# Kernel optimization log

Hardware: AMD Instinct MI355X
Metric: run time of the kernel (lower is better)

Reference implementation:

```python
import jax, jax.numpy as jnp
from jax import lax
import numpy as np

# FlowNetC correlation configuration (matches init_kwargs)
PAD = 20          # pad_size
K = 1             # kernel_size (kernel_radius = 0)
MAX_DISP = 20     # max_displacement
S1 = 1            # stride1
S2 = 2            # stride2
R = MAX_DISP // S2          # neighborhood_grid_radius = 10
GW = 2 * R + 1              # neighborhood_grid_width = 21
NOUT = GW * GW              # 441 output planes


def setup_inputs() -> dict:
    key = jax.random.key(0)
    k1, k2 = jax.random.split(key)
    B, C, H, W = 8, 256, 96, 128
    return {
        "input1": jax.random.normal(k1, (B, C, H, W), dtype=jnp.float32),
        "input2": jax.random.normal(k2, (B, C, H, W), dtype=jnp.float32),
    }


def _correlation(input1, input2):
    B, C, H, W = input1.shape
    # pad second input; with kernel_size=1 and pad==max_displacement the
    # output grid is exactly the input grid, and displaced pixel (y+dy, x+dx)
    # lives at padded index (y + PAD + dy, x + PAD + dx).
    p2 = jnp.pad(input2, ((0, 0), (0, 0), (PAD, PAD), (PAD, PAD)))
    sumelems = jnp.asarray(K * K * C, dtype=input1.dtype)

    def body(o):
        # displacement (dy, dx) = ((o//GW - R)*S2, (o%GW - R)*S2);
        # slice start in padded coords = PAD + d = (o//GW)*S2, (o%GW)*S2
        dy = (o // GW) * S2
        dx = (o % GW) * S2
        sl = lax.dynamic_slice(p2, (0, 0, dy, dx), (B, C, H, W))
        return jnp.einsum('bchw,bchw->bhw', input1, sl) / sumelems

    out = lax.map(body, jnp.arange(NOUT))       # [441, B, H, W]
    return jnp.transpose(out, (1, 0, 2, 3))     # [B, 441, H, W]


def reference(input1, input2):
    return _correlation(input1, input2)
```

## Files before the change

### kernel.cpp

```cpp
#include <hip/hip_runtime.h>
#include <hip/hip_bf16.h>


typedef __attribute__((ext_vector_type(8))) short bf16x8;
typedef __attribute__((ext_vector_type(4))) float f32x4;
typedef __attribute__((ext_vector_type(4))) unsigned u32x4;

constexpr int Bn = 8, Cn = 256, Hn = 96, Wn = 128, GW = 21;
constexpr int KC = 32, NCH = Cn / KC;
constexpr int NWG = Bn * Hn * GW;
constexpr int JW = 23;
constexpr size_t TELEMS = (size_t)Bn * Hn * NCH * 2048;

__device__ inline unsigned pack_bf16(float lo, float hi) {
    __hip_bfloat16 l = __float2bfloat16(lo);
    __hip_bfloat16 h = __float2bfloat16(hi);
    unsigned short lu, hu;
    __builtin_memcpy(&lu, &l, 2);
    __builtin_memcpy(&hu, &h, 2);
    return (unsigned)lu | ((unsigned)hu << 16);
}

__global__ __launch_bounds__(256) void prepack(
    const float* __restrict__ in1, const float* __restrict__ in2,
    unsigned* __restrict__ T)
{
    unsigned u = blockIdx.x;
    int ch = u & 7;  u >>= 3;
    int y  = u % 96; u /= 96;
    int b  = u & 7;  u >>= 3;
    const float* src = u ? in2 : in1;

    int t  = threadIdx.x;
    int tm = t & 63;
    int tg = t >> 6;

    const size_t chw = (size_t)Hn * Wn;
    const float* p = src + ((size_t)(b * Cn + ch * 32 + 8 * tg)) * chw
                         + (size_t)y * Wn + 2 * tm;
    float2 f[8];
#pragma unroll
    for (int k = 0; k < 8; ++k)
        f[k] = *(const float2*)(p + (size_t)k * chw);

    u32x4 ae, ao;
#pragma unroll
    for (int ku = 0; ku < 4; ++ku) {
        ae[ku] = pack_bf16(f[2 * ku].x, f[2 * ku + 1].x);
        ao[ku] = pack_bf16(f[2 * ku].y, f[2 * ku + 1].y);
    }
    unsigned* To = T + u * TELEMS + ((size_t)(b * Hn + y) * NCH + ch) * 2048
                     + ((tm >> 4) * 4 + tg) * 64 + (tm & 15) * 4;
    *(u32x4*)(To)        = ae;
    *(u32x4*)(To + 1024) = ao;
}

__global__ __launch_bounds__(256) void corr_frag(
    const unsigned* __restrict__ T1, const unsigned* __restrict__ T2,
    float* __restrict__ out)
{
    __shared__ float sout[Wn * JW];

    int orig = blockIdx.x;
    int xcd  = orig & 7;
    int i    = orig >> 3;
    int yw   = i % 3;  int t = i / 3;
    int dyi  = t % 21; t /= 21;
    int sub  = t & 1;
    int par  = (t >> 1) & 1;
    int b    = t >> 2;
    int y    = 12 * xcd + par + 2 * (3 * sub + yw);

    int y2  = y + 2 * dyi - 20;
    bool y2ok = (y2 >= 0) && (y2 < Hn);

    int tid = threadIdx.x;
    int w   = tid >> 6;
    int l   = tid & 63;
    int p   = w >> 1;
    int h   = w & 1;
    int g   = l >> 4;
    int m16 = l & 15;

    f32x4 acc[2][4] = {};

    if (y2ok) {
        const unsigned* pa = T1 + (size_t)(b * Hn + y)  * (NCH * 2048)
                                + p * 1024 + g * 64 + m16 * 4;
        const unsigned* pb = T2 + (size_t)(b * Hn + y2) * (NCH * 2048)
                                + p * 1024 + g * 64 + m16 * 4 + h * 256;

        bf16x8 ca0, ca1, cb0, cb1, cb2;
        ca0 = *(const bf16x8*)(pa + (2 * h + 0) * 256);
        ca1 = *(const bf16x8*)(pa + (2 * h + 1) * 256);
        cb0 = *(const bf16x8*)(pb + 0 * 256);
        cb1 = *(const bf16x8*)(pb + 1 * 256);
        cb2 = *(const bf16x8*)(pb + 2 * 256);

        for (int ch = 0; ch < NCH; ++ch) {
            bf16x8 na0, na1, nb0, nb1, nb2;
            if (ch + 1 < NCH) {
                const unsigned* A = pa + (ch + 1) * 2048;
                const unsigned* B = pb + (ch + 1) * 2048;
                na0 = *(const bf16x8*)(A + (2 * h + 0) * 256);
                na1 = *(const bf16x8*)(A + (2 * h + 1) * 256);
                nb0 = *(const bf16x8*)(B + 0 * 256);
                nb1 = *(const bf16x8*)(B + 1 * 256);
                nb2 = *(const bf16x8*)(B + 2 * 256);
            }
            if (h == 0) {
                acc[0][0] = __builtin_amdgcn_mfma_f32_16x16x32_bf16(ca0, cb0, acc[0][0], 0, 0, 0);
                acc[0][1] = __builtin_amdgcn_mfma_f32_16x16x32_bf16(ca0, cb1, acc[0][1], 0, 0, 0);
                acc[1][0] = __builtin_amdgcn_mfma_f32_16x16x32_bf16(ca1, cb0, acc[1][0], 0, 0, 0);
                acc[1][1] = __builtin_amdgcn_mfma_f32_16x16x32_bf16(ca1, cb1, acc[1][1], 0, 0, 0);
                acc[1][2] = __builtin_amdgcn_mfma_f32_16x16x32_bf16(ca1, cb2, acc[1][2], 0, 0, 0);
            } else {
                acc[0][1] = __builtin_amdgcn_mfma_f32_16x16x32_bf16(ca0, cb0, acc[0][1], 0, 0, 0);
                acc[0][2] = __builtin_amdgcn_mfma_f32_16x16x32_bf16(ca0, cb1, acc[0][2], 0, 0, 0);
                acc[0][3] = __builtin_amdgcn_mfma_f32_16x16x32_bf16(ca0, cb2, acc[0][3], 0, 0, 0);
                acc[1][2] = __builtin_amdgcn_mfma_f32_16x16x32_bf16(ca1, cb1, acc[1][2], 0, 0, 0);
                acc[1][3] = __builtin_amdgcn_mfma_f32_16x16x32_bf16(ca1, cb2, acc[1][3], 0, 0, 0);
            }
            ca0 = na0; ca1 = na1;
            cb0 = nb0; cb1 = nb1; cb2 = nb2;
        }
    }

    for (int i2 = tid; i2 < Wn * JW; i2 += 256) sout[i2] = 0.0f;
    __syncthreads();

    if (y2ok) {
        const float scale = 1.0f / 256.0f;
#pragma unroll
        for (int a = 0; a < 2; ++a)
#pragma unroll
            for (int n = 0; n < 4; ++n)
#pragma unroll
                for (int r = 0; r < 4; ++r) {
                    int xp = (2 * h + a) * 16 + g * 4 + r;
                    int up = n * 16 + m16;
                    int j  = up - xp + 10;
                    if ((unsigned)j < 21u)
                        sout[(2 * xp + p) * JW + j] = acc[a][n][r] * scale;
                }
    }
    __syncthreads();

    unsigned base0 = (unsigned)(((b * (GW * GW) + dyi * GW) * Hn + y) * Wn);
    constexpr unsigned PLANE = (unsigned)(Hn * Wn);
    for (int s = tid; s < GW * Wn; s += 256) {
        int j = s >> 7;
        int x = s & 127;
        out[base0 + (unsigned)j * PLANE + (unsigned)x] = sout[x * JW + j];
    }
}

__device__ inline void lds_barrier() {
    asm volatile("s_waitcnt lgkmcnt(0)" ::: "memory");
    __builtin_amdgcn_s_barrier();
    __builtin_amdgcn_sched_barrier(0);
}

__global__ __launch_bounds__(256) void corr_mfma_fb(
    const float* __restrict__ in1, const float* __restrict__ in2,
    float* __restrict__ out)
{
    __shared__ unsigned lds[4][1024];
    int orig = blockIdx.x;
    int xcd  = orig & 7;
    int i    = orig >> 3;
    int yw   = i % 3;  int t = i / 3;
    int dyi  = t % 21; t /= 21;
    int sub  = t & 1;
    int par  = (t >> 1) & 1;
    int b    = t >> 2;
    int y    = 12 * xcd + par + 2 * (3 * sub + yw);
    int y2  = y + 2 * dyi - 20;
    bool y2ok = (y2 >= 0) && (y2 < Hn);

    int tid = threadIdx.x;
    int w   = tid >> 6;
    int l   = tid & 63;
    int p   = w >> 1;
    int h   = w & 1;
    int g   = l >> 4;
    int m16 = l & 15;

    const size_t chw = (size_t)Hn * Wn;
    const float* pA = in1 + ((size_t)b * Cn) * chw + (size_t)y * Wn;
    const float* pB = in2 + ((size_t)b * Cn) * chw + (size_t)(y2ok ? y2 : 0) * Wn;

    int tm = tid & 63;
    int tg = tid >> 6;
    const int loff = ((tm >> 4) * 4 + tg) * 64 + (tm & 15) * 4;

    f32x4 acc[2][4] = {};
    float ax[8], ay[8], bx[8], by[8];

    auto prefetch = [&](int chunk) {
        size_t base = (size_t)(chunk * KC + 8 * tg) * chw + 2 * tm;
#pragma unroll
        for (int k = 0; k < 8; ++k) {
            float2 tA = *(const float2*)(pA + base + (size_t)k * chw);
            float2 tB = *(const float2*)(pB + base + (size_t)k * chw);
            ax[k] = tA.x; ay[k] = tA.y;
            bx[k] = tB.x; by[k] = tB.y;
        }
        __builtin_amdgcn_sched_barrier(0);
    };
    auto writeout = [&]() {
#pragma unroll
        for (int k = 0; k < 8; ++k)
            asm volatile("" : "+v"(ax[k]), "+v"(ay[k]), "+v"(bx[k]), "+v"(by[k]));
        u32x4 ae, ao, be, bo;
#pragma unroll
        for (int ku = 0; ku < 4; ++ku) {
            ae[ku] = pack_bf16(ax[2 * ku], ax[2 * ku + 1]);
            ao[ku] = pack_bf16(ay[2 * ku], ay[2 * ku + 1]);
            be[ku] = pack_bf16(bx[2 * ku], bx[2 * ku + 1]);
            bo[ku] = pack_bf16(by[2 * ku], by[2 * ku + 1]);
        }
        *(u32x4*)&lds[0][loff] = ae;
        *(u32x4*)&lds[1][loff] = ao;
        *(u32x4*)&lds[2][loff] = be;
        *(u32x4*)&lds[3][loff] = bo;
    };
    auto compute = [&]() {
        const unsigned* Pa = &lds[p][0];
        const unsigned* Pb = &lds[2 + p][0];
        int fo = g * 64 + m16 * 4;
        bf16x8 A0  = *(const bf16x8*)(Pa + (2 * h + 0) * 256 + fo);
        bf16x8 A1  = *(const bf16x8*)(Pa + (2 * h + 1) * 256 + fo);
        bf16x8 Bf0 = *(const bf16x8*)(Pb + 0 * 256 + fo);
        bf16x8 Bf1 = *(const bf16x8*)(Pb + 1 * 256 + fo);
        bf16x8 Bf2 = *(const bf16x8*)(Pb + 2 * 256 + fo);
        bf16x8 Bf3 = *(const bf16x8*)(Pb + 3 * 256 + fo);
        acc[0][0] = __builtin_amdgcn_mfma_f32_16x16x32_bf16(A0, Bf0, acc[0][0], 0, 0, 0);
        acc[0][1] = __builtin_amdgcn_mfma_f32_16x16x32_bf16(A0, Bf1, acc[0][1], 0, 0, 0);
        acc[0][2] = __builtin_amdgcn_mfma_f32_16x16x32_bf16(A0, Bf2, acc[0][2], 0, 0, 0);
        acc[0][3] = __builtin_amdgcn_mfma_f32_16x16x32_bf16(A0, Bf3, acc[0][3], 0, 0, 0);
        acc[1][0] = __builtin_amdgcn_mfma_f32_16x16x32_bf16(A1, Bf0, acc[1][0], 0, 0, 0);
        acc[1][1] = __builtin_amdgcn_mfma_f32_16x16x32_bf16(A1, Bf1, acc[1][1], 0, 0, 0);
        acc[1][2] = __builtin_amdgcn_mfma_f32_16x16x32_bf16(A1, Bf2, acc[1][2], 0, 0, 0);
        acc[1][3] = __builtin_amdgcn_mfma_f32_16x16x32_bf16(A1, Bf3, acc[1][3], 0, 0, 0);
    };

    if (y2ok) {
        prefetch(0);
        for (int it = 0; it < NCH; ++it) {
            writeout();
            lds_barrier();
            if (it + 1 < NCH) prefetch(it + 1);
            compute();
            lds_barrier();
        }
    }

    __syncthreads();
    float* sout = (float*)&lds[0][0];
    for (int i2 = tid; i2 < Wn * JW; i2 += 256) sout[i2] = 0.0f;
    __syncthreads();
    if (y2ok) {
        const float scale = 1.0f / 256.0f;
#pragma unroll
        for (int a = 0; a < 2; ++a)
#pragma unroll
            for (int n = 0; n < 4; ++n)
#pragma unroll
                for (int r = 0; r < 4; ++r) {
                    int xp = (2 * h + a) * 16 + g * 4 + r;
                    int up = n * 16 + m16;
                    int j  = up - xp + 10;
                    if ((unsigned)j < 21u)
                        sout[(2 * xp + p) * JW + j] = acc[a][n][r] * scale;
                }
    }
    __syncthreads();
    unsigned base0 = (unsigned)(((b * (GW * GW) + dyi * GW) * Hn + y) * Wn);
    constexpr unsigned PLANE = (unsigned)(Hn * Wn);
    for (int s = tid; s < GW * Wn; s += 256) {
        int j = s >> 7;
        int x = s & 127;
        out[base0 + (unsigned)j * PLANE + (unsigned)x] = sout[x * JW + j];
    }
}

extern "C" void kernel_launch(void* const* d_in, const int* in_sizes, int n_in,
                              void* d_out, int out_size, void* d_ws, size_t ws_size,
                              hipStream_t stream) {
    const float* in1 = (const float*)d_in[0];
    const float* in2 = (const float*)d_in[1];
    float* out = (float*)d_out;
    size_t need = 2 * TELEMS * sizeof(unsigned);
    if (ws_size >= need) {
        unsigned* T = (unsigned*)d_ws;
        prepack<<<2 * Bn * Hn * NCH, 256, 0, stream>>>(in1, in2, T);
        corr_frag<<<NWG, 256, 0, stream>>>(T, T + TELEMS, out);
    } else {
        corr_mfma_fb<<<NWG, 256, 0, stream>>>(in1, in2, out);
    }
}
```

Baseline: 172.3 us.

## Process three vertical displacements per workgroup to reuse input1 fragments

Each workgroup now computes three dy displacements instead of one, so the input1 fragment loads are shared across three sets of input2 rows and the grid shrinks threefold. The software prefetch of the next channel chunk is removed in favour of direct loads inside the loop. Out-of-range rows are clamped to row 0 and still run their MFMAs, while the write-out is serialised through shared memory three times per block. Accumulator register use triples, which may reduce occupancy.

```diff
diff --git a/kernel.cpp b/kernel.cpp
--- a/kernel.cpp
+++ b/kernel.cpp
@@ -8,7 +8,9 @@
 
 constexpr int Bn = 8, Cn = 256, Hn = 96, Wn = 128, GW = 21;
 constexpr int KC = 32, NCH = Cn / KC;
-constexpr int NWG = Bn * Hn * GW;
+constexpr int NDG = 7;
+constexpr int NWG3 = Bn * Hn * NDG;
+constexpr int NWGFB = Bn * Hn * GW;
 constexpr int JW = 23;
 constexpr size_t TELEMS = (size_t)Bn * Hn * NCH * 2048;
 
@@ -55,7 +57,7 @@
     *(u32x4*)(To + 1024) = ao;
 }
 
-__global__ __launch_bounds__(256) void corr_frag(
+__global__ __launch_bounds__(256) void corr_frag3(
     const unsigned* __restrict__ T1, const unsigned* __restrict__ T2,
     float* __restrict__ out)
 {
@@ -65,14 +67,19 @@
     int xcd  = orig & 7;
     int i    = orig >> 3;
     int yw   = i % 3;  int t = i / 3;
-    int dyi  = t % 21; t /= 21;
+    int dg   = t % NDG; t /= NDG;
     int sub  = t & 1;
     int par  = (t >> 1) & 1;
     int b    = t >> 2;
     int y    = 12 * xcd + par + 2 * (3 * sub + yw);
 
-    int y2  = y + 2 * dyi - 20;
-    bool y2ok = (y2 >= 0) && (y2 < Hn);
+    int rowv[3], y2c[3];
+#pragma unroll
+    for (int d = 0; d < 3; ++d) {
+        int y2 = y + 2 * (3 * dg + d) - 20;
+        rowv[d] = (y2 >= 0) && (y2 < Hn);
+        y2c[d]  = rowv[d] ? y2 : 0;
+    }
 
     int tid = threadIdx.x;
     int w   = tid >> 6;
@@ -82,76 +89,74 @@
     int g   = l >> 4;
     int m16 = l & 15;
 
-    f32x4 acc[2][4] = {};
-
-    if (y2ok) {
-        const unsigned* pa = T1 + (size_t)(b * Hn + y)  * (NCH * 2048)
+    f32x4 acc[3][2][4] = {};
+
+    {
+        const unsigned* pa = T1 + (size_t)(b * Hn + y) * (NCH * 2048)
                                 + p * 1024 + g * 64 + m16 * 4;
-        const unsigned* pb = T2 + (size_t)(b * Hn + y2) * (NCH * 2048)
-                                + p * 1024 + g * 64 + m16 * 4 + h * 256;
-
-        bf16x8 ca0, ca1, cb0, cb1, cb2;
-        ca0 = *(const bf16x8*)(pa + (2 * h + 0) * 256);
-        ca1 = *(const bf16x8*)(pa + (2 * h + 1) * 256);
-        cb0 = *(const bf16x8*)(pb + 0 * 256);
-        cb1 = *(const bf16x8*)(pb + 1 * 256);
-        cb2 = *(const bf16x8*)(pb + 2 * 256);
+        const unsigned* pb0 = T2 + (size_t)(b * Hn + y2c[0]) * (NCH * 2048)
+                                 + p * 1024 + g * 64 + m16 * 4 + h * 256;
+        const unsigned* pb1 = T2 + (size_t)(b * Hn + y2c[1]) * (NCH * 2048)
+                                 + p * 1024 + g * 64 + m16 * 4 + h * 256;
+        const unsigned* pb2 = T2 + (size_t)(b * Hn + y2c[2]) * (NCH * 2048)
+                                 + p * 1024 + g * 64 + m16 * 4 + h * 256;
 
         for (int ch = 0; ch < NCH; ++ch) {
-            bf16x8 na0, na1, nb0, nb1, nb2;
-            if (ch + 1 < NCH) {
-                const unsigned* A = pa + (ch + 1) * 2048;
-                const unsigned* B = pb + (ch + 1) * 2048;
-                na0 = *(const bf16x8*)(A + (2 * h + 0) * 256);
-                na1 = *(const bf16x8*)(A + (2 * h + 1) * 256);
-                nb0 = *(const bf16x8*)(B + 0 * 256);
-                nb1 = *(const bf16x8*)(B + 1 * 256);
-                nb2 = *(const bf16x8*)(B + 2 * 256);
+            const unsigned* A = pa + ch * 2048;
+            bf16x8 a0 = *(const bf16x8*)(A + (2 * h + 0) * 256);
+            bf16x8 a1 = *(const bf16x8*)(A + (2 * h + 1) * 256);
+#pragma unroll
+            for (int d = 0; d < 3; ++d) {
+                const unsigned* B = (d == 0 ? pb0 : (d == 1 ? pb1 : pb2)) + ch * 2048;
+                bf16x8 b0 = *(const bf16x8*)(B + 0 * 256);
+                bf16x8 b1 = *(const bf16x8*)(B + 1 * 256);
+                bf16x8 b2 = *(const bf16x8*)(B + 2 * 256);
+                if (h == 0) {
+                    acc[d][0][0] = __builtin_amdgcn_mfma_f32_16x16x32_bf16(a0, b0, acc[d][0][0], 0, 0, 0);
+                    acc[d][0][1] = __builtin_amdgcn_mfma_f32_16x16x32_bf16(a0, b1, acc[d][0][1], 0, 0, 0);
+                    acc[d][1][0] = __builtin_amdgcn_mfma_f32_16x16x32_bf16(a1, b0, acc[d][1][0], 0, 0, 0);
+                    acc[d][1][1] = __builtin_amdgcn_mfma_f32_16x16x32_bf16(a1, b1, acc[d][1][1], 0, 0, 0);
+                    acc[d][1][2] = __builtin_amdgcn_mfma_f32_16x16x32_bf16(a1, b2, acc[d][1][2], 0, 0, 0);
+                } else {
+                    acc[d][0][1] = __builtin_amdgcn_mfma_f32_16x16x32_bf16(a0, b0, acc[d][0][1], 0, 0, 0);
+                    acc[d][0][2] = __builtin_amdgcn_mfma_f32_16x16x32_bf16(a0, b1, acc[d][0][2], 0, 0, 0);
+                    acc[d][0][3] = __builtin_amdgcn_mfma_f32_16x16x32_bf16(a0, b2, acc[d][0][3], 0, 0, 0);
+                    acc[d][1][2] = __builtin_amdgcn_mfma_f32_16x16x32_bf16(a1, b1, acc[d][1][2], 0, 0, 0);
+                    acc[d][1][3] = __builtin_amdgcn_mfma_f32_16x16x32_bf16(a1, b2, acc[d][1][3], 0, 0, 0);
+                }
             }
-            if (h == 0) {
-                acc[0][0] = __builtin_amdgcn_mfma_f32_16x16x32_bf16(ca0, cb0, acc[0][0], 0, 0, 0);
-                acc[0][1] = __builtin_amdgcn_mfma_f32_16x16x32_bf16(ca0, cb1, acc[0][1], 0, 0, 0);
-                acc[1][0] = __builtin_amdgcn_mfma_f32_16x16x32_bf16(ca1, cb0, acc[1][0], 0, 0, 0);
-                acc[1][1] = __builtin_amdgcn_mfma_f32_16x16x32_bf16(ca1, cb1, acc[1][1], 0, 0, 0);
-                acc[1][2] = __builtin_amdgcn_mfma_f32_16x16x32_bf16(ca1, cb2, acc[1][2], 0, 0, 0);
-            } else {
-                acc[0][1] = __builtin_amdgcn_mfma_f32_16x16x32_bf16(ca0, cb0, acc[0][1], 0, 0, 0);
-                acc[0][2] = __builtin_amdgcn_mfma_f32_16x16x32_bf16(ca0, cb1, acc[0][2], 0, 0, 0);
-                acc[0][3] = __builtin_amdgcn_mfma_f32_16x16x32_bf16(ca0, cb2, acc[0][3], 0, 0, 0);
-                acc[1][2] = __builtin_amdgcn_mfma_f32_16x16x32_bf16(ca1, cb1, acc[1][2], 0, 0, 0);
-                acc[1][3] = __builtin_amdgcn_mfma_f32_16x16x32_bf16(ca1, cb2, acc[1][3], 0, 0, 0);
-            }
-            ca0 = na0; ca1 = na1;
-            cb0 = nb0; cb1 = nb1; cb2 = nb2;
-        }
-    }
-
-    for (int i2 = tid; i2 < Wn * JW; i2 += 256) sout[i2] = 0.0f;
-    __syncthreads();
-
-    if (y2ok) {
-        const float scale = 1.0f / 256.0f;
-#pragma unroll
-        for (int a = 0; a < 2; ++a)
-#pragma unroll
-            for (int n = 0; n < 4; ++n)
-#pragma unroll
-                for (int r = 0; r < 4; ++r) {
-                    int xp = (2 * h + a) * 16 + g * 4 + r;
-                    int up = n * 16 + m16;
-                    int j  = up - xp + 10;
-                    if ((unsigned)j < 21u)
-                        sout[(2 * xp + p) * JW + j] = acc[a][n][r] * scale;
-                }
-    }
-    __syncthreads();
-
-    unsigned base0 = (unsigned)(((b * (GW * GW) + dyi * GW) * Hn + y) * Wn);
+        }
+    }
+
+    const float scale = 1.0f / 256.0f;
     constexpr unsigned PLANE = (unsigned)(Hn * Wn);
-    for (int s = tid; s < GW * Wn; s += 256) {
-        int j = s >> 7;
-        int x = s & 127;
-        out[base0 + (unsigned)j * PLANE + (unsigned)x] = sout[x * JW + j];
+
+#pragma unroll
+    for (int d = 0; d < 3; ++d) {
+        __syncthreads();
+        for (int i2 = tid; i2 < Wn * JW; i2 += 256) sout[i2] = 0.0f;
+        __syncthreads();
+        if (rowv[d]) {
+#pragma unroll
+            for (int a = 0; a < 2; ++a)
+#pragma unroll
+                for (int n = 0; n < 4; ++n)
+#pragma unroll
+                    for (int r = 0; r < 4; ++r) {
+                        int xp = (2 * h + a) * 16 + g * 4 + r;
+                        int up = n * 16 + m16;
+                        int j  = up - xp + 10;
+                        if ((unsigned)j < 21u)
+                            sout[(2 * xp + p) * JW + j] = acc[d][a][n][r] * scale;
+                    }
+        }
+        __syncthreads();
+        unsigned base0 = (unsigned)(((b * (GW * GW) + (3 * dg + d) * GW) * Hn + y) * Wn);
+        for (int s = tid; s < GW * Wn; s += 256) {
+            int j = s >> 7;
+            int x = s & 127;
+            out[base0 + (unsigned)j * PLANE + (unsigned)x] = sout[x * JW + j];
+        }
     }
 }
 
@@ -295,8 +300,8 @@
     if (ws_size >= need) {
         unsigned* T = (unsigned*)d_ws;
         prepack<<<2 * Bn * Hn * NCH, 256, 0, stream>>>(in1, in2, T);
-        corr_frag<<<NWG, 256, 0, stream>>>(T, T + TELEMS, out);
+        corr_frag3<<<NWG3, 256, 0, stream>>>(T, T + TELEMS, out);
     } else {
-        corr_mfma_fb<<<NWG, 256, 0, stream>>>(in1, in2, out);
-    }
-}
+        corr_mfma_fb<<<NWGFB, 256, 0, stream>>>(in1, in2, out);
+    }
+}
```

Result: slower. 204.4 us (+18.7%).
